# Kernel optimization log

Measured on AMD Instinct MI355X. Metric: run time of the kernel, lower is better.

## Reference

```python
import jax, jax.numpy as jnp
import numpy as np

B, I, D = 2048, 4096, 512          # batch of candidates, num rated items, item_dim
IE, UE = 512, 1024                 # item_emb, user_emb
D1, D2, D3 = 1024, 512, 256        # MLP dense widths


def setup_inputs() -> dict:
    key = jax.random.key(0)
    ks = jax.random.split(key, 16)
    s = 0.02  # weight init scale
    candidate_items = jax.random.normal(ks[0], (B, D), dtype=jnp.float32)
    rated_items = jax.random.normal(ks[1], (I, D), dtype=jnp.float32)
    ratings = jax.random.uniform(ks[2], (B, I), dtype=jnp.float32, minval=0.5, maxval=5.0)
    keep = jax.random.uniform(ks[3], (B, I)) < 0.05
    user_matrix = jnp.where(keep, ratings, 0.0)
    return dict(
        candidate_items=candidate_items,
        rated_items=rated_items,
        user_matrix=user_matrix,
        att_w=jax.random.normal(ks[4], (2 * D, 1), dtype=jnp.float32) * s,
        att_b=jnp.zeros((1,), jnp.float32),
        iw1=jax.random.normal(ks[5], (D, 2 * IE), dtype=jnp.float32) * s,
        ib1=jnp.zeros((2 * IE,), jnp.float32),
        iw2=jax.random.normal(ks[6], (2 * IE, IE), dtype=jnp.float32) * s,
        ib2=jnp.zeros((IE,), jnp.float32),
        uw1=jax.random.normal(ks[7], (D, 2 * UE), dtype=jnp.float32) * s,
        ub1=jnp.zeros((2 * UE,), jnp.float32),
        uw2=jax.random.normal(ks[8], (2 * UE, UE), dtype=jnp.float32) * s,
        ub2=jnp.zeros((UE,), jnp.float32),
        mw1=jax.random.normal(ks[9], (IE + UE, D1), dtype=jnp.float32) * s,
        mb1=jnp.zeros((D1,), jnp.float32),
        mw2=jax.random.normal(ks[10], (D1, D2), dtype=jnp.float32) * s,
        mb2=jnp.zeros((D2,), jnp.float32),
        mw3=jax.random.normal(ks[11], (D2, D3), dtype=jnp.float32) * s,
        mb3=jnp.zeros((D3,), jnp.float32),
        mw4=jax.random.normal(ks[12], (D3, 1), dtype=jnp.float32) * s,
        mb4=jnp.zeros((1,), jnp.float32),
    )


def reference(candidate_items, rated_items, user_matrix,
              att_w, att_b, iw1, ib1, iw2, ib2, uw1, ub1, uw2, ub2,
              mw1, mb1, mw2, mb2, mw3, mb3, mw4, mb4):
    d = candidate_items.shape[1]
    # AttentionNet(Linear(2D,1)) on cat(cand_repeat, rated_tile) decomposes exactly:
    # score[b,i] = cand[b] @ w_c + rated[i] @ w_r + b  (same math, no (B*I,2D) blowup)
    wc, wr = att_w[:d], att_w[d:]                      # (D,1), (D,1)
    scores = candidate_items @ wc + (rated_items @ wr).T + att_b  # (B, I)
    scores = jnp.where(user_matrix == 0.0, -jnp.inf, scores)
    att = jax.nn.softmax(scores, axis=1)
    att = jnp.nan_to_num(att, nan=0.0, posinf=0.0, neginf=0.0)  # rows with no ratings -> 0
    user_feat = (att * user_matrix) @ rated_items      # (B, D)
    # dual towers (dropout = identity in eval)
    item_emb = jax.nn.relu(jax.nn.relu(candidate_items @ iw1 + ib1) @ iw2 + ib2)
    user_emb = jax.nn.relu(jax.nn.relu(user_feat @ uw1 + ub1) @ uw2 + ub2)
    x = jnp.concatenate([item_emb, user_emb], axis=1)  # (B, IE+UE)
    x = jax.nn.relu(x @ mw1 + mb1)
    x = jax.nn.relu(x @ mw2 + mb2)
    x = jax.nn.relu(x @ mw3 + mb3)
    return x @ mw4 + mb4                               # (B, 1)
```

## Files before the change

### kernel.cpp

```cpp
#include <hip/hip_runtime.h>
#include <cstddef>

constexpr int Bn = 2048;
constexpr int In = 4096;
constexpr int Dn = 512;

typedef _Float16 f16;
typedef _Float16 f16x8 __attribute__((ext_vector_type(8)));
typedef float    f32x4 __attribute__((ext_vector_type(4)));

__global__ __launch_bounds__(256) void k_rs(const float* __restrict__ rated,
                                            const float* __restrict__ att_w,
                                            float* __restrict__ rs) {
  const int wid  = threadIdx.x >> 6;
  const int lane = threadIdx.x & 63;
  const int i = blockIdx.x * 4 + wid;
  const float* row = rated + (size_t)i * Dn;
  const float* wr  = att_w + Dn;
  float s = 0.f;
  #pragma unroll
  for (int d = 0; d < Dn / 64; ++d)
    s = fmaf(row[lane + d * 64], wr[lane + d * 64], s);
  #pragma unroll
  for (int off = 32; off > 0; off >>= 1) s += __shfl_down(s, off);
  if (lane == 0) rs[i] = s;
}

__global__ __launch_bounds__(256) void k_att(const float* __restrict__ um,
                                             const float* __restrict__ rs,
                                             f16* __restrict__ att) {
  __shared__ float t[In];
  __shared__ float red[4];
  const int tid = threadIdx.x;
  const int b = blockIdx.x;
  const float* umrow = um + (size_t)b * In;

  float ua[16];
  float lmax = -INFINITY;
  #pragma unroll
  for (int it = 0; it < 4; ++it) {
    const int i = (it * 256 + tid) * 4;
    const float4 v = *reinterpret_cast<const float4*>(umrow + i);
    ua[it * 4 + 0] = v.x; ua[it * 4 + 1] = v.y;
    ua[it * 4 + 2] = v.z; ua[it * 4 + 3] = v.w;
    #pragma unroll
    for (int j = 0; j < 4; ++j) {
      if (ua[it * 4 + j] != 0.f) {
        const float r = rs[i + j];
        t[i + j] = r;
        lmax = fmaxf(lmax, r);
      } else {
        t[i + j] = -INFINITY;
      }
    }
  }
  #pragma unroll
  for (int off = 32; off > 0; off >>= 1) lmax = fmaxf(lmax, __shfl_down(lmax, off));
  if ((tid & 63) == 0) red[tid >> 6] = lmax;
  __syncthreads();
  const float m = fmaxf(fmaxf(red[0], red[1]), fmaxf(red[2], red[3]));
  __syncthreads();

  float lsum = 0.f;
  #pragma unroll
  for (int it = 0; it < 4; ++it) {
    const int i = (it * 256 + tid) * 4;
    #pragma unroll
    for (int j = 0; j < 4; ++j) {
      float v = 0.f;
      if (ua[it * 4 + j] != 0.f) {
        const float e = __expf(t[i + j] - m);
        lsum += e;
        v = e * ua[it * 4 + j];
      }
      t[i + j] = v;
    }
  }
  #pragma unroll
  for (int off = 32; off > 0; off >>= 1) lsum += __shfl_down(lsum, off);
  if ((tid & 63) == 0) red[tid >> 6] = lsum;
  __syncthreads();
  const float S = red[0] + red[1] + red[2] + red[3];
  const float inv = (S > 0.f) ? 1.0f / S : 0.0f;

  f16* arow = att + (size_t)b * In;
  #pragma unroll
  for (int it = 0; it < 2; ++it) {
    const int i = (it * 256 + tid) * 8;
    f16x8 h;
    #pragma unroll
    for (int j = 0; j < 8; ++j) h[j] = (f16)(t[i + j] * inv);
    *reinterpret_cast<f16x8*>(arow + i) = h;
  }
}

__global__ __launch_bounds__(256) void k_transpose_f2h(const float* __restrict__ src,
                                                       f16* __restrict__ dst,
                                                       int K, int N) {
  __shared__ float tile[32][33];
  const int tx = threadIdx.x & 31;
  const int ty = threadIdx.x >> 5;
  const int n0 = blockIdx.x * 32;
  const int k0 = blockIdx.y * 32;
  #pragma unroll
  for (int i = 0; i < 4; ++i)
    tile[ty + i * 8][tx] = src[(size_t)(k0 + ty + i * 8) * N + n0 + tx];
  __syncthreads();
  #pragma unroll
  for (int i = 0; i < 4; ++i)
    dst[(size_t)(n0 + ty + i * 8) * K + k0 + tx] = (f16)tile[tx][ty + i * 8];
}

__global__ __launch_bounds__(256) void k_cast_f2h(const float* __restrict__ src,
                                                  f16* __restrict__ dst, int n) {
  const int i = (blockIdx.x * 256 + threadIdx.x) * 4;
  if (i < n) {
    const float4 v = *reinterpret_cast<const float4*>(src + i);
    f16 h0 = (f16)v.x, h1 = (f16)v.y, h2 = (f16)v.z, h3 = (f16)v.w;
    f16* p = dst + i;
    p[0] = h0; p[1] = h1; p[2] = h2; p[3] = h3;
  }
}

template <bool RELU, bool BIAS>
__global__ __launch_bounds__(256) void k_hgemm(const f16* __restrict__ A,
                                               const f16* __restrict__ Wt,
                                               const float* __restrict__ bias,
                                               f16* __restrict__ C, int ldc,
                                               int N, int K) {
  __shared__ __align__(16) f16 As[64][72];
  __shared__ __align__(16) f16 Bs[64][72];

  const int tid  = threadIdx.x;
  const int lane = tid & 63;
  const int wave = tid >> 6;
  const int wrow = (wave >> 1) * 32;
  const int wcol = (wave & 1) * 32;
  const int lrow = lane & 15;
  const int koff = (lane >> 4) * 8;

  const int bm = blockIdx.y * 64;
  const int bn = blockIdx.x * 64;

  const int r = tid >> 2;
  const int c = (tid & 3) * 16;

  const f16* pa = A  + (size_t)(bm + r) * K + c;
  const f16* pb = Wt + (size_t)(bn + r) * K + c;

  f16x8 ra0, ra1, rb0, rb1;
  #define LOADG()                                                   \
    ra0 = *reinterpret_cast<const f16x8*>(pa + 0);                  \
    ra1 = *reinterpret_cast<const f16x8*>(pa + 8);                  \
    rb0 = *reinterpret_cast<const f16x8*>(pb + 0);                  \
    rb1 = *reinterpret_cast<const f16x8*>(pb + 8);

  f32x4 acc[2][2] = {};

  LOADG();
  for (int k0 = 0; k0 < K; k0 += 64) {
    *reinterpret_cast<f16x8*>(&As[r][c + 0]) = ra0;
    *reinterpret_cast<f16x8*>(&As[r][c + 8]) = ra1;
    *reinterpret_cast<f16x8*>(&Bs[r][c + 0]) = rb0;
    *reinterpret_cast<f16x8*>(&Bs[r][c + 8]) = rb1;
    __syncthreads();

    if (k0 + 64 < K) {
      pa += 64; pb += 64;
      LOADG();
    }

    #pragma unroll
    for (int ks = 0; ks < 2; ++ks) {
      const int kk = ks * 32 + koff;
      const f16x8 a0 = *reinterpret_cast<const f16x8*>(&As[wrow +  0 + lrow][kk]);
      const f16x8 a1 = *reinterpret_cast<const f16x8*>(&As[wrow + 16 + lrow][kk]);
      const f16x8 b0 = *reinterpret_cast<const f16x8*>(&Bs[wcol +  0 + lrow][kk]);
      const f16x8 b1 = *reinterpret_cast<const f16x8*>(&Bs[wcol + 16 + lrow][kk]);

      acc[0][0] = __builtin_amdgcn_mfma_f32_16x16x32_f16(a0, b0, acc[0][0], 0, 0, 0);
      acc[0][1] = __builtin_amdgcn_mfma_f32_16x16x32_f16(a0, b1, acc[0][1], 0, 0, 0);
      acc[1][0] = __builtin_amdgcn_mfma_f32_16x16x32_f16(a1, b0, acc[1][0], 0, 0, 0);
      acc[1][1] = __builtin_amdgcn_mfma_f32_16x16x32_f16(a1, b1, acc[1][1], 0, 0, 0);
    }
    __syncthreads();
  }
  #undef LOADG

  const int orow = (lane >> 4) * 4;
  #pragma unroll
  for (int mf = 0; mf < 2; ++mf)
    #pragma unroll
    for (int nf = 0; nf < 2; ++nf) {
      const int col = bn + wcol + nf * 16 + lrow;
      const float bv = BIAS ? bias[col] : 0.f;
      #pragma unroll
      for (int rr = 0; rr < 4; ++rr) {
        const int row = bm + wrow + mf * 16 + orow + rr;
        float v = acc[mf][nf][rr] + bv;
        if (RELU) v = fmaxf(v, 0.f);
        C[(size_t)row * ldc + col] = (f16)v;
      }
    }
}

__global__ __launch_bounds__(256) void k_final(const f16* __restrict__ h3,
                                               const float* __restrict__ mw4,
                                               const float* __restrict__ mb4,
                                               float* __restrict__ out) {
  const int wid = threadIdx.x >> 6;
  const int lane = threadIdx.x & 63;
  const int row = blockIdx.x * 4 + wid;
  const f16* hr = h3 + (size_t)row * 256;
  float s = 0.f;
  #pragma unroll
  for (int d = 0; d < 4; ++d)
    s = fmaf((float)hr[lane + d * 64], mw4[lane + d * 64], s);
  #pragma unroll
  for (int off = 32; off > 0; off >>= 1) s += __shfl_down(s, off);
  if (lane == 0) out[row] = s + mb4[0];
}

extern "C" void kernel_launch(void* const* d_in, const int* in_sizes, int n_in,
                              void* d_out, int out_size, void* d_ws, size_t ws_size,
                              hipStream_t stream) {
  const float* cand  = (const float*)d_in[0];
  const float* rated = (const float*)d_in[1];
  const float* um    = (const float*)d_in[2];
  const float* att_w = (const float*)d_in[3];
  const float* iw1 = (const float*)d_in[5];
  const float* ib1 = (const float*)d_in[6];
  const float* iw2 = (const float*)d_in[7];
  const float* ib2 = (const float*)d_in[8];
  const float* uw1 = (const float*)d_in[9];
  const float* ub1 = (const float*)d_in[10];
  const float* uw2 = (const float*)d_in[11];
  const float* ub2 = (const float*)d_in[12];
  const float* mw1 = (const float*)d_in[13];
  const float* mb1 = (const float*)d_in[14];
  const float* mw2 = (const float*)d_in[15];
  const float* mb2 = (const float*)d_in[16];
  const float* mw3 = (const float*)d_in[17];
  const float* mb3 = (const float*)d_in[18];
  const float* mw4 = (const float*)d_in[19];
  const float* mb4 = (const float*)d_in[20];
  float* out = (float*)d_out;

  f16*   hws = (f16*)d_ws;
  float* rs  = (float*)d_ws;
  size_t off = 8192;
  auto take = [&](size_t n) { f16* p = hws + off; off += n; return p; };
  f16* t_iw1   = take(512 * 1024);
  f16* t_iw2   = take(1024 * 512);
  f16* t_uw1   = take(512 * 2048);
  f16* t_uw2   = take(2048 * 1024);
  f16* t_mw1   = take(1536 * 1024);
  f16* t_mw2   = take(1024 * 512);
  f16* t_mw3   = take(512 * 256);
  f16* t_rated = take(512 * 4096);
  f16* cand_h  = take(2048 * 512);
  f16* uf_h    = take(2048 * 512);
  f16* big     = take(2048 * 2048);
  f16* Xc      = take(2048 * 1536);
  f16* spare   = take(2048 * 512);
  (void)spare;
  f16* att_d = big;
  f16* h_i1 = big;
  f16* h_u1 = big;
  f16* h_m1 = big;
  f16* h_m2 = uf_h;
  f16* h_m3 = cand_h;

  dim3 blk(256);

  k_rs<<<dim3(In / 4), blk, 0, stream>>>(rated, att_w, rs);
  k_att<<<dim3(Bn), blk, 0, stream>>>(um, rs, att_d);

  k_transpose_f2h<<<dim3( 512/32, 4096/32), blk, 0, stream>>>(rated, t_rated, 4096, 512);
  k_transpose_f2h<<<dim3(1024/32,  512/32), blk, 0, stream>>>(iw1, t_iw1,  512, 1024);
  k_transpose_f2h<<<dim3( 512/32, 1024/32), blk, 0, stream>>>(iw2, t_iw2, 1024,  512);
  k_transpose_f2h<<<dim3(2048/32,  512/32), blk, 0, stream>>>(uw1, t_uw1,  512, 2048);
  k_transpose_f2h<<<dim3(1024/32, 2048/32), blk, 0, stream>>>(uw2, t_uw2, 2048, 1024);
  k_transpose_f2h<<<dim3(1024/32, 1536/32), blk, 0, stream>>>(mw1, t_mw1, 1536, 1024);
  k_transpose_f2h<<<dim3( 512/32, 1024/32), blk, 0, stream>>>(mw2, t_mw2, 1024,  512);
  k_transpose_f2h<<<dim3( 256/32,  512/32), blk, 0, stream>>>(mw3, t_mw3,  512,  256);
  k_cast_f2h<<<dim3(Bn * Dn / 1024), blk, 0, stream>>>(cand, cand_h, Bn * Dn);

  k_hgemm<false, false><<<dim3(512/64, Bn/64), blk, 0, stream>>>(
      att_d, t_rated, nullptr, uf_h, 512, 512, 4096);

  k_hgemm<true, true><<<dim3(1024/64, Bn/64), blk, 0, stream>>>(cand_h, t_iw1, ib1, h_i1, 1024, 1024, 512);
  k_hgemm<true, true><<<dim3( 512/64, Bn/64), blk, 0, stream>>>(h_i1,   t_iw2, ib2, Xc,   1536,  512, 1024);

  k_hgemm<true, true><<<dim3(2048/64, Bn/64), blk, 0, stream>>>(uf_h, t_uw1, ub1, h_u1,     2048, 2048, 512);
  k_hgemm<true, true><<<dim3(1024/64, Bn/64), blk, 0, stream>>>(h_u1, t_uw2, ub2, Xc + 512, 1536, 1024, 2048);

  k_hgemm<true, true><<<dim3(1024/64, Bn/64), blk, 0, stream>>>(Xc,   t_mw1, mb1, h_m1, 1024, 1024, 1536);
  k_hgemm<true, true><<<dim3( 512/64, Bn/64), blk, 0, stream>>>(h_m1, t_mw2, mb2, h_m2,  512,  512, 1024);
  k_hgemm<true, true><<<dim3( 256/64, Bn/64), blk, 0, stream>>>(h_m2, t_mw3, mb3, h_m3,  256,  256, 512);

  k_final<<<dim3(Bn / 4), blk, 0, stream>>>(h_m3, mw4, mb4, out);
}
```

Baseline: 290.4 us.

## Split-K GEMMs with reduce kernels and co-schedule independent tower GEMMs

Replaces the templated GEMM with a descriptor-driven kernel that can run two independent GEMMs in one launch (e.g. user-feature GEMM alongside item tower layer 1). It also splits K across blocks for the small-N layers and writes fp32 partials, which a separate reduce kernel sums before applying bias and ReLU. The aim is to fill the GPU with more blocks for layers whose 64x64 tile grid is too small, and to overlap independent work. The cost is extra fp32 partial traffic through global memory and additional reduce launches.

```diff
diff --git a/kernel.cpp b/kernel.cpp
--- a/kernel.cpp
+++ b/kernel.cpp
@@ -122,12 +122,26 @@
   }
 }
 
-template <bool RELU, bool BIAS>
-__global__ __launch_bounds__(256) void k_hgemm(const f16* __restrict__ A,
-                                               const f16* __restrict__ Wt,
-                                               const float* __restrict__ bias,
-                                               f16* __restrict__ C, int ldc,
-                                               int N, int K) {
+struct GemmDesc {
+  const f16* A;
+  const f16* Wt;
+  const float* bias;
+  f16* C;
+  float* P;
+  int N, K, Kc, ldc, nTilesN, relu;
+};
+
+__global__ __launch_bounds__(256) void k_mgemm(GemmDesc dA, GemmDesc dB, int bSplit) {
+  const bool second = ((int)blockIdx.x >= bSplit);
+  const GemmDesc d = second ? dB : dA;
+  const int local = second ? (int)blockIdx.x - bSplit : (int)blockIdx.x;
+
+  const int bm = (local & 31) * 64;
+  const int rest = local >> 5;
+  const int bn = (rest % d.nTilesN) * 64;
+  const int ks = rest / d.nTilesN;
+  const int kBeg = ks * d.Kc;
+
   __shared__ __align__(16) f16 As[64][72];
   __shared__ __align__(16) f16 Bs[64][72];
 
@@ -139,14 +153,11 @@
   const int lrow = lane & 15;
   const int koff = (lane >> 4) * 8;
 
-  const int bm = blockIdx.y * 64;
-  const int bn = blockIdx.x * 64;
-
   const int r = tid >> 2;
   const int c = (tid & 3) * 16;
 
-  const f16* pa = A  + (size_t)(bm + r) * K + c;
-  const f16* pb = Wt + (size_t)(bn + r) * K + c;
+  const f16* pa = d.A  + (size_t)(bm + r) * d.K + kBeg + c;
+  const f16* pb = d.Wt + (size_t)(bn + r) * d.K + kBeg + c;
 
   f16x8 ra0, ra1, rb0, rb1;
   #define LOADG()                                                   \
@@ -158,21 +169,21 @@
   f32x4 acc[2][2] = {};
 
   LOADG();
-  for (int k0 = 0; k0 < K; k0 += 64) {
+  for (int k0 = 0; k0 < d.Kc; k0 += 64) {
     *reinterpret_cast<f16x8*>(&As[r][c + 0]) = ra0;
     *reinterpret_cast<f16x8*>(&As[r][c + 8]) = ra1;
     *reinterpret_cast<f16x8*>(&Bs[r][c + 0]) = rb0;
     *reinterpret_cast<f16x8*>(&Bs[r][c + 8]) = rb1;
     __syncthreads();
 
-    if (k0 + 64 < K) {
+    if (k0 + 64 < d.Kc) {
       pa += 64; pb += 64;
       LOADG();
     }
 
     #pragma unroll
-    for (int ks = 0; ks < 2; ++ks) {
-      const int kk = ks * 32 + koff;
+    for (int kss = 0; kss < 2; ++kss) {
+      const int kk = kss * 32 + koff;
       const f16x8 a0 = *reinterpret_cast<const f16x8*>(&As[wrow +  0 + lrow][kk]);
       const f16x8 a1 = *reinterpret_cast<const f16x8*>(&As[wrow + 16 + lrow][kk]);
       const f16x8 b0 = *reinterpret_cast<const f16x8*>(&Bs[wcol +  0 + lrow][kk]);
@@ -188,20 +199,67 @@
   #undef LOADG
 
   const int orow = (lane >> 4) * 4;
-  #pragma unroll
-  for (int mf = 0; mf < 2; ++mf)
-    #pragma unroll
-    for (int nf = 0; nf < 2; ++nf) {
-      const int col = bn + wcol + nf * 16 + lrow;
-      const float bv = BIAS ? bias[col] : 0.f;
+  if (d.P) {
+    float* pp = d.P + (size_t)ks * ((size_t)2048 * d.N);
+    #pragma unroll
+    for (int mf = 0; mf < 2; ++mf)
       #pragma unroll
-      for (int rr = 0; rr < 4; ++rr) {
-        const int row = bm + wrow + mf * 16 + orow + rr;
-        float v = acc[mf][nf][rr] + bv;
-        if (RELU) v = fmaxf(v, 0.f);
-        C[(size_t)row * ldc + col] = (f16)v;
+      for (int nf = 0; nf < 2; ++nf) {
+        const int col = bn + wcol + nf * 16 + lrow;
+        #pragma unroll
+        for (int rr = 0; rr < 4; ++rr) {
+          const int row = bm + wrow + mf * 16 + orow + rr;
+          pp[(size_t)row * d.N + col] = acc[mf][nf][rr];
+        }
       }
-    }
+  } else {
+    #pragma unroll
+    for (int mf = 0; mf < 2; ++mf)
+      #pragma unroll
+      for (int nf = 0; nf < 2; ++nf) {
+        const int col = bn + wcol + nf * 16 + lrow;
+        const float bv = d.bias ? d.bias[col] : 0.f;
+        #pragma unroll
+        for (int rr = 0; rr < 4; ++rr) {
+          const int row = bm + wrow + mf * 16 + orow + rr;
+          float v = acc[mf][nf][rr] + bv;
+          if (d.relu) v = fmaxf(v, 0.f);
+          d.C[(size_t)row * d.ldc + col] = (f16)v;
+        }
+      }
+  }
+}
+
+__global__ __launch_bounds__(256) void k_reduce(const float* __restrict__ P,
+                                                int S, int MN, int N,
+                                                const float* __restrict__ bias,
+                                                int relu, f16* __restrict__ C,
+                                                int ldc) {
+  const int idx = (blockIdx.x * 256 + threadIdx.x) * 8;
+  float v[8];
+  {
+    const float4 a0 = *reinterpret_cast<const float4*>(P + idx);
+    const float4 a1 = *reinterpret_cast<const float4*>(P + idx + 4);
+    v[0] = a0.x; v[1] = a0.y; v[2] = a0.z; v[3] = a0.w;
+    v[4] = a1.x; v[5] = a1.y; v[6] = a1.z; v[7] = a1.w;
+  }
+  for (int s = 1; s < S; ++s) {
+    const float* ps = P + (size_t)s * MN + idx;
+    const float4 b0 = *reinterpret_cast<const float4*>(ps);
+    const float4 b1 = *reinterpret_cast<const float4*>(ps + 4);
+    v[0] += b0.x; v[1] += b0.y; v[2] += b0.z; v[3] += b0.w;
+    v[4] += b1.x; v[5] += b1.y; v[6] += b1.z; v[7] += b1.w;
+  }
+  const int row = idx / N;
+  const int col = idx % N;
+  f16x8 h;
+  #pragma unroll
+  for (int j = 0; j < 8; ++j) {
+    float x = v[j] + (bias ? bias[col + j] : 0.f);
+    if (relu) x = fmaxf(x, 0.f);
+    h[j] = (f16)x;
+  }
+  *reinterpret_cast<f16x8*>(C + (size_t)row * ldc + col) = h;
 }
 
 __global__ __launch_bounds__(256) void k_final(const f16* __restrict__ h3,
@@ -263,9 +321,10 @@
   f16* big     = take(2048 * 2048);
   f16* Xc      = take(2048 * 1536);
   f16* spare   = take(2048 * 512);
+  f16* h_i1b   = take(2048 * 1024);
+  float* Pbuf  = (float*)take(8 * 1024 * 1024);
   (void)spare;
   f16* att_d = big;
-  f16* h_i1 = big;
   f16* h_u1 = big;
   f16* h_m1 = big;
   f16* h_m2 = uf_h;
@@ -286,18 +345,31 @@
   k_transpose_f2h<<<dim3( 256/32,  512/32), blk, 0, stream>>>(mw3, t_mw3,  512,  256);
   k_cast_f2h<<<dim3(Bn * Dn / 1024), blk, 0, stream>>>(cand, cand_h, Bn * Dn);
 
-  k_hgemm<false, false><<<dim3(512/64, Bn/64), blk, 0, stream>>>(
-      att_d, t_rated, nullptr, uf_h, 512, 512, 4096);
-
-  k_hgemm<true, true><<<dim3(1024/64, Bn/64), blk, 0, stream>>>(cand_h, t_iw1, ib1, h_i1, 1024, 1024, 512);
-  k_hgemm<true, true><<<dim3( 512/64, Bn/64), blk, 0, stream>>>(h_i1,   t_iw2, ib2, Xc,   1536,  512, 1024);
-
-  k_hgemm<true, true><<<dim3(2048/64, Bn/64), blk, 0, stream>>>(uf_h, t_uw1, ub1, h_u1,     2048, 2048, 512);
-  k_hgemm<true, true><<<dim3(1024/64, Bn/64), blk, 0, stream>>>(h_u1, t_uw2, ub2, Xc + 512, 1536, 1024, 2048);
-
-  k_hgemm<true, true><<<dim3(1024/64, Bn/64), blk, 0, stream>>>(Xc,   t_mw1, mb1, h_m1, 1024, 1024, 1536);
-  k_hgemm<true, true><<<dim3( 512/64, Bn/64), blk, 0, stream>>>(h_m1, t_mw2, mb2, h_m2,  512,  512, 1024);
-  k_hgemm<true, true><<<dim3( 256/64, Bn/64), blk, 0, stream>>>(h_m2, t_mw3, mb3, h_m3,  256,  256, 512);
+  GemmDesc dUF = { att_d, t_rated, nullptr, nullptr, Pbuf, 512, 4096, 1024, 512, 8, 0 };
+  GemmDesc dI1 = { cand_h, t_iw1, ib1, h_i1b, nullptr, 1024, 512, 512, 1024, 16, 1 };
+  GemmDesc dU1 = { uf_h, t_uw1, ub1, h_u1, nullptr, 2048, 512, 512, 2048, 32, 1 };
+  GemmDesc dI2 = { h_i1b, t_iw2, ib2, Xc, nullptr, 512, 1024, 1024, 1536, 8, 1 };
+  GemmDesc dU2 = { h_u1, t_uw2, nullptr, nullptr, Pbuf, 1024, 2048, 1024, 1536, 16, 1 };
+  GemmDesc dM1 = { Xc, t_mw1, nullptr, nullptr, Pbuf, 1024, 1536, 768, 1024, 16, 1 };
+  GemmDesc dM2 = { h_m1, t_mw2, nullptr, nullptr, Pbuf, 512, 1024, 256, 512, 8, 1 };
+  GemmDesc dM3 = { h_m2, t_mw3, nullptr, nullptr, Pbuf, 256, 512, 128, 256, 4, 1 };
+
+  k_mgemm<<<dim3(1536), blk, 0, stream>>>(dUF, dI1, 1024);
+  k_reduce<<<dim3(512), blk, 0, stream>>>(Pbuf, 4, 2048 * 512, 512, nullptr, 0, uf_h, 512);
+
+  k_mgemm<<<dim3(1280), blk, 0, stream>>>(dU1, dI2, 1024);
+
+  k_mgemm<<<dim3(1024), blk, 0, stream>>>(dU2, dU2, 1024);
+  k_reduce<<<dim3(1024), blk, 0, stream>>>(Pbuf, 2, 2048 * 1024, 1024, ub2, 1, Xc + 512, 1536);
+
+  k_mgemm<<<dim3(1024), blk, 0, stream>>>(dM1, dM1, 1024);
+  k_reduce<<<dim3(1024), blk, 0, stream>>>(Pbuf, 2, 2048 * 1024, 1024, mb1, 1, h_m1, 1024);
+
+  k_mgemm<<<dim3(1024), blk, 0, stream>>>(dM2, dM2, 1024);
+  k_reduce<<<dim3(512), blk, 0, stream>>>(Pbuf, 4, 2048 * 512, 512, mb2, 1, h_m2, 512);
+
+  k_mgemm<<<dim3(512), blk, 0, stream>>>(dM3, dM3, 512);
+  k_reduce<<<dim3(256), blk, 0, stream>>>(Pbuf, 4, 2048 * 256, 256, mb3, 1, h_m3, 256);
 
   k_final<<<dim3(Bn / 4), blk, 0, stream>>>(h_m3, mw4, mb4, out);
 }
```

New measurement: 292.7 us. Within noise of the previous version (+0.8%).
